# Kernel optimization log

Hardware: AMD Instinct MI355X
Metric: run time of the kernel (lower is better)

The kernel has to match this reference:

```python
import jax, jax.numpy as jnp
import numpy as np

H, Hk, Hv, Dk, Dv, K = 1536, 8, 16, 64, 64, 4
KEY_DIM = Hk * Dk            # 512
VALUE_DIM = Hv * Dv          # 1024
CONV_DIM = 2 * KEY_DIM + VALUE_DIM  # 2048


def setup_inputs() -> dict:
    key = jax.random.key(0)
    ks = jax.random.split(key, 12)
    s = 0.02
    return {
        "hidden_states": jax.random.normal(ks[0], (1, H, 1, 1), jnp.float32),
        "W_qkv": jax.random.normal(ks[1], (CONV_DIM, H), jnp.float32) * s,
        "W_z": jax.random.normal(ks[2], (VALUE_DIM, H), jnp.float32) * s,
        "W_a": jax.random.normal(ks[3], (Hv, H), jnp.float32) * s,
        "W_b": jax.random.normal(ks[4], (Hv, H), jnp.float32) * s,
        "W_out": jax.random.normal(ks[5], (H, VALUE_DIM), jnp.float32) * s,
        "conv1d_weight": jax.random.normal(ks[6], (CONV_DIM, K), jnp.float32) * 0.1,
        "A_log": jax.random.normal(ks[7], (Hv,), jnp.float32) * 0.1,
        "dt_bias": jax.random.normal(ks[8], (Hv,), jnp.float32) * 0.1,
        "norm_weight": jnp.ones((Dv,), jnp.float32),
        "state": jax.random.normal(ks[9], (1, Hv, Dk, Dv), jnp.float32) * 0.05,
        "conv_cache": jax.random.normal(ks[10], (1, CONV_DIM, K - 1), jnp.float32) * 0.1,
    }


def _l2n(t):
    # l2_normalize with eps=1e-12 (matches torch rsqrt(sum(x^2)+eps))
    return t * jax.lax.rsqrt(jnp.sum(t * t, axis=-1, keepdims=True) + 1e-12)


def reference(hidden_states, W_qkv, W_z, W_a, W_b, W_out, conv1d_weight,
              A_log, dt_bias, norm_weight, state, conv_cache):
    x = hidden_states.reshape(-1)                       # [H]
    qkv = W_qkv @ x                                     # [CONV_DIM]
    z = (W_z @ x).reshape(Hv, Dv)                       # gate, [Hv, Dv]
    a = W_a @ x                                         # [Hv]
    beta = jax.nn.sigmoid(W_b @ x)                      # [Hv]

    # causal conv as weighted sum over cache + current token
    combined = jnp.concatenate([conv_cache[0], qkv[:, None]], axis=1)  # [CONV_DIM, K]
    conv_out = jax.nn.silu(jnp.sum(combined * conv1d_weight, axis=1))  # [CONV_DIM]

    q = conv_out[:KEY_DIM].reshape(Hk, Dk)
    k = conv_out[KEY_DIM:2 * KEY_DIM].reshape(Hk, Dk)
    v = conv_out[2 * KEY_DIM:].reshape(Hv, Dv)

    rep = Hv // Hk                                      # kv_group = 2
    q = jnp.repeat(q, rep, axis=0)                      # [Hv, Dk]
    k = jnp.repeat(k, rep, axis=0)
    q = _l2n(q) * (Dk ** -0.5)
    k = _l2n(k)

    # gated decay
    g = -jnp.exp(A_log) * jax.nn.softplus(a + dt_bias)  # [Hv]
    st = state[0] * jnp.exp(g)[:, None, None]           # [Hv, Dk, Dv]

    # delta-rule update
    retrieved = jnp.einsum('hkv,hk->hv', st, k)         # [Hv, Dv]
    delta = (v - retrieved) * beta[:, None]             # [Hv, Dv]
    new_state = st + jnp.einsum('hk,hv->hkv', k, delta) # [Hv, Dk, Dv]

    out = jnp.einsum('hkv,hk->hv', new_state, q)        # [Hv, Dv]

    # gated RMSNorm over Dv
    var = jnp.mean(out * out, axis=-1, keepdims=True)
    out = norm_weight * (out * jax.lax.rsqrt(var + 1e-6)) * jax.nn.silu(z)

    y = W_out @ out.reshape(-1)                         # [H]
    return y.reshape(1, -1, 1, 1)
```

## Files before the change

### kernel.cpp

```cpp
#include <hip/hip_runtime.h>

#define H 1536
#define HK 8
#define HV 16
#define DK 64
#define DV 64
#define KEY_DIM 512
#define VALUE_DIM 1024
#define CONV_DIM 2048
#define NROWS1 (CONV_DIM + VALUE_DIM + HV + HV)
#define NBLK 256

__device__ unsigned g_ticket = 0;

__device__ __forceinline__ float wave_reduce_sum(float v) {
#pragma unroll
    for (int off = 32; off > 0; off >>= 1) v += __shfl_xor(v, off, 64);
    return v;
}

__device__ __forceinline__ float dot4(float4 a, float4 b) {
    return a.x * b.x + a.y * b.y + a.z * b.z + a.w * b.w;
}

__device__ __forceinline__ void grid_barrier() {
    __syncthreads();
    if (threadIdx.x == 0) {
        unsigned t = __hip_atomic_fetch_add(&g_ticket, 1u, __ATOMIC_ACQ_REL,
                                            __HIP_MEMORY_SCOPE_AGENT);
        unsigned target = (t / NBLK + 1u) * NBLK;
        while (__hip_atomic_load(&g_ticket, __ATOMIC_ACQUIRE,
                                 __HIP_MEMORY_SCOPE_AGENT) < target)
            __builtin_amdgcn_s_sleep(2);
    }
    __syncthreads();
}

__global__ __launch_bounds__(256) void fused_decode(
        const float* __restrict__ x,
        const float* __restrict__ Wqkv, const float* __restrict__ Wz,
        const float* __restrict__ Wa,   const float* __restrict__ Wb,
        const float* __restrict__ Wout,
        const float* __restrict__ conv_w, const float* __restrict__ conv_cache,
        const float* __restrict__ A_log, const float* __restrict__ dt_bias,
        const float* __restrict__ norm_w,
        const float* __restrict__ state,
        float* __restrict__ ws,
        float* __restrict__ og,
        float* __restrict__ y) {
    const int tid  = threadIdx.x;
    const int lane = tid & 63;
    const int wv   = tid >> 6;
    const int blk  = blockIdx.x;
    const int wg   = blk * 4 + wv;

    __shared__ float s_state[DK * DV];
    __shared__ float q_s[64], k_s[64], v_s[64];
    __shared__ float red_r[256], red_o[256];
    __shared__ float scal[3];

    if (blk < HV) {
        const float4* st4 = (const float4*)(state + (size_t)blk * DK * DV);
        float4* ss4 = (float4*)s_state;
#pragma unroll
        for (int j = 0; j < 4; ++j) ss4[tid + 256 * j] = st4[tid + 256 * j];
    }

    float4 wo0[4], wo1[4] = {};
    {
        const float4* w4 = (const float4*)(Wout + (size_t)wg * VALUE_DIM);
#pragma unroll
        for (int j = 0; j < 4; ++j) wo0[j] = w4[lane + 64 * j];
    }
    if (wg < 512) {
        const float4* w4 = (const float4*)(Wout + (size_t)(1024 + wg) * VALUE_DIM);
#pragma unroll
        for (int j = 0; j < 4; ++j) wo1[j] = w4[lane + 64 * j];
    }

    auto rowptr = [&](int row) -> const float* {
        if (row < CONV_DIM)                  return Wqkv + (size_t)row * H;
        if (row < CONV_DIM + VALUE_DIM)      return Wz + (size_t)(row - CONV_DIM) * H;
        if (row < CONV_DIM + VALUE_DIM + HV) return Wa + (size_t)(row - CONV_DIM - VALUE_DIM) * H;
        return Wb + (size_t)(row - CONV_DIM - VALUE_DIM - HV) * H;
    };
    const int r0 = wg * 3;
    const float4* wA = (const float4*)rowptr(r0);
    const float4* wB = (const float4*)rowptr(r0 + 1);
    const float4* wC = (const float4*)rowptr(r0 + 2);
    const bool extra = (wv == 0) && (blk >= 208) && (blk < 240);
    const int erow = 3072 + blk - 208;
    const float4* wD = (const float4*)rowptr(extra ? erow : r0);
    const float4* x4 = (const float4*)x;

    float a0 = 0.f, a1 = 0.f, a2 = 0.f, a3 = 0.f;
#pragma unroll
    for (int j = 0; j < 6; ++j) {
        const int idx = lane + 64 * j;
        const float4 xb = x4[idx];
        a0 += dot4(wA[idx], xb);
        a1 += dot4(wB[idx], xb);
        a2 += dot4(wC[idx], xb);
        if (extra) a3 += dot4(wD[idx], xb);
    }
    a0 = wave_reduce_sum(a0);
    a1 = wave_reduce_sum(a1);
    a2 = wave_reduce_sum(a2);
    if (lane == 0) { ws[r0] = a0; ws[r0 + 1] = a1; ws[r0 + 2] = a2; }
    if (extra) {
        a3 = wave_reduce_sum(a3);
        if (lane == 0) ws[erow] = a3;
    }

    grid_barrier();

    if (blk < HV) {
        const int h = blk;
        const int grp = wv;
        if (grp < 3) {
            int i;
            if (grp == 0)      i = (h >> 1) * 64 + lane;
            else if (grp == 1) i = KEY_DIM + (h >> 1) * 64 + lane;
            else               i = 2 * KEY_DIM + h * 64 + lane;
            float raw = conv_cache[i * 3 + 0] * conv_w[i * 4 + 0]
                      + conv_cache[i * 3 + 1] * conv_w[i * 4 + 1]
                      + conv_cache[i * 3 + 2] * conv_w[i * 4 + 2]
                      + ws[i]                 * conv_w[i * 4 + 3];
            float c = raw / (1.f + expf(-raw));
            if (grp == 2) {
                v_s[lane] = c;
            } else {
                float ss  = wave_reduce_sum(c * c);
                float inv = rsqrtf(ss + 1e-12f);
                if (grp == 0) q_s[lane] = c * inv * 0.125f;
                else          k_s[lane] = c * inv;
            }
        } else if (lane == 0) {
            float aa = ws[CONV_DIM + VALUE_DIM + h] + dt_bias[h];
            float sp = (aa > 20.f) ? aa : log1pf(expf(aa));
            scal[0] = expf(-expf(A_log[h]) * sp);
            float braw = ws[CONV_DIM + VALUE_DIM + HV + h];
            scal[1] = 1.f / (1.f + expf(-braw));
        }
        __syncthreads();

        float pr = 0.f, po = 0.f;
        const int k0 = grp * 16;
#pragma unroll
        for (int kk = 0; kk < 16; ++kk) {
            float s = s_state[(k0 + kk) * 64 + lane];
            pr += s * k_s[k0 + kk];
            po += s * q_s[k0 + kk];
        }
        red_r[tid] = pr;
        red_o[tid] = po;
        if (grp == 0) {
            float t = wave_reduce_sum(k_s[lane] * q_s[lane]);
            if (lane == 0) scal[2] = t;
        }
        __syncthreads();

        if (tid < 64) {
            const float decay = scal[0], beta = scal[1], kq = scal[2];
            float r = (red_r[tid] + red_r[64 + tid] + red_r[128 + tid] + red_r[192 + tid]) * decay;
            float o = (red_o[tid] + red_o[64 + tid] + red_o[128 + tid] + red_o[192 + tid]) * decay;
            float delta = (v_s[tid] - r) * beta;
            float outv  = o + delta * kq;
            float ss  = wave_reduce_sum(outv * outv);
            float inv = rsqrtf(ss * (1.f / 64.f) + 1e-6f);
            float zz  = ws[CONV_DIM + h * 64 + tid];
            float gate = zz / (1.f + expf(-zz));
            og[h * 64 + tid] = norm_w[tid] * outv * inv * gate;
        }
    }

    grid_barrier();

    const float4* og4 = (const float4*)og;
    const float4 g0 = og4[lane];
    const float4 g1 = og4[lane + 64];
    const float4 g2 = og4[lane + 128];
    const float4 g3 = og4[lane + 192];
    float acc = dot4(wo0[0], g0) + dot4(wo0[1], g1) + dot4(wo0[2], g2) + dot4(wo0[3], g3);
    acc = wave_reduce_sum(acc);
    if (lane == 0) y[wg] = acc;
    if (wg < 512) {
        float acc2 = dot4(wo1[0], g0) + dot4(wo1[1], g1) + dot4(wo1[2], g2) + dot4(wo1[3], g3);
        acc2 = wave_reduce_sum(acc2);
        if (lane == 0) y[1024 + wg] = acc2;
    }
}

extern "C" void kernel_launch(void* const* d_in, const int* in_sizes, int n_in,
                              void* d_out, int out_size, void* d_ws, size_t ws_size,
                              hipStream_t stream) {
    const float* x     = (const float*)d_in[0];
    const float* Wqkv  = (const float*)d_in[1];
    const float* Wz    = (const float*)d_in[2];
    const float* Wa    = (const float*)d_in[3];
    const float* Wb    = (const float*)d_in[4];
    const float* Wout  = (const float*)d_in[5];
    const float* convw = (const float*)d_in[6];
    const float* Alog  = (const float*)d_in[7];
    const float* dtb   = (const float*)d_in[8];
    const float* normw = (const float*)d_in[9];
    const float* state = (const float*)d_in[10];
    const float* cch   = (const float*)d_in[11];

    float* ws = (float*)d_ws;
    float* og = ws + NROWS1;
    float* y  = (float*)d_out;

    fused_decode<<<NBLK, 256, 0, stream>>>(x, Wqkv, Wz, Wa, Wb, Wout, convw, cch,
                                           Alog, dtb, normw, state, ws, og, y);
}
```

Before: 120.3 us.

## Split grid barrier into flag-based phases and move decode heads to tail blocks

Replaces the ticket-counter grid barrier with separate arrival counters and release flags. Only the 16 decode blocks wait for the first phase, while all blocks wait on a second flag that the decode blocks alone signal. The W_a and W_b projections move into the decode blocks, which now sit at the last 16 block indices, and their results stay in shared memory. All weight, x, conv and state loads are issued into registers before the dot products, to raise memory-level parallelism. This lowers barrier traffic and idle waiting, at the cost of more register pressure and an epoch scheme that relies on the counters' low bits lining up across launches.

```diff
diff --git a/kernel.cpp b/kernel.cpp
--- a/kernel.cpp
+++ b/kernel.cpp
@@ -8,35 +8,28 @@
 #define KEY_DIM 512
 #define VALUE_DIM 1024
 #define CONV_DIM 2048
-#define NROWS1 (CONV_DIM + VALUE_DIM + HV + HV)
+#define NROWS1 3104
 #define NBLK 256
-
-__device__ unsigned g_ticket = 0;
+#define DEC0 240
+
+struct BarrierState {
+    alignas(128) unsigned cnt1;
+    alignas(128) unsigned flag1;
+    alignas(128) unsigned cnt2;
+    alignas(128) unsigned flag2;
+};
+__device__ BarrierState g_bar;
 
 __device__ __forceinline__ float wave_reduce_sum(float v) {
 #pragma unroll
     for (int off = 32; off > 0; off >>= 1) v += __shfl_xor(v, off, 64);
     return v;
 }
-
 __device__ __forceinline__ float dot4(float4 a, float4 b) {
     return a.x * b.x + a.y * b.y + a.z * b.z + a.w * b.w;
 }
 
-__device__ __forceinline__ void grid_barrier() {
-    __syncthreads();
-    if (threadIdx.x == 0) {
-        unsigned t = __hip_atomic_fetch_add(&g_ticket, 1u, __ATOMIC_ACQ_REL,
-                                            __HIP_MEMORY_SCOPE_AGENT);
-        unsigned target = (t / NBLK + 1u) * NBLK;
-        while (__hip_atomic_load(&g_ticket, __ATOMIC_ACQUIRE,
-                                 __HIP_MEMORY_SCOPE_AGENT) < target)
-            __builtin_amdgcn_s_sleep(2);
-    }
-    __syncthreads();
-}
-
-__global__ __launch_bounds__(256) void fused_decode(
+__global__ __launch_bounds__(256, 1) void fused_decode(
         const float* __restrict__ x,
         const float* __restrict__ Wqkv, const float* __restrict__ Wz,
         const float* __restrict__ Wa,   const float* __restrict__ Wb,
@@ -53,99 +46,128 @@
     const int wv   = tid >> 6;
     const int blk  = blockIdx.x;
     const int wg   = blk * 4 + wv;
+    const int hblk = blk - DEC0;
+    const bool isdec = (hblk >= 0);
 
     __shared__ float s_state[DK * DV];
     __shared__ float q_s[64], k_s[64], v_s[64];
     __shared__ float red_r[256], red_o[256];
     __shared__ float scal[3];
-
-    if (blk < HV) {
-        const float4* st4 = (const float4*)(state + (size_t)blk * DK * DV);
-        float4* ss4 = (float4*)s_state;
-#pragma unroll
-        for (int j = 0; j < 4; ++j) ss4[tid + 256 * j] = st4[tid + 256 * j];
-    }
-
-    float4 wo0[4], wo1[4] = {};
+    __shared__ float s_ab[2];
+
+    const float4* x4 = (const float4*)x;
+    const int r0 = wg * 3;
+    const float4* wA = (const float4*)((r0   < CONV_DIM) ? Wqkv + (size_t)r0*H       : Wz + (size_t)(r0-CONV_DIM)*H);
+    const float4* wB = (const float4*)((r0+1 < CONV_DIM) ? Wqkv + (size_t)(r0+1)*H   : Wz + (size_t)(r0+1-CONV_DIM)*H);
+    const float4* wC = (const float4*)((r0+2 < CONV_DIM) ? Wqkv + (size_t)(r0+2)*H   : Wz + (size_t)(r0+2-CONV_DIM)*H);
+
+    float4 rx[6], rA[6], rB[6], rC[6];
+#pragma unroll
+    for (int j = 0; j < 6; ++j) rx[j] = x4[lane + 64*j];
+#pragma unroll
+    for (int j = 0; j < 6; ++j) rA[j] = wA[lane + 64*j];
+#pragma unroll
+    for (int j = 0; j < 6; ++j) rB[j] = wB[lane + 64*j];
+#pragma unroll
+    for (int j = 0; j < 6; ++j) rC[j] = wC[lane + 64*j];
+
+    float4 wo0[4], wo1[4];
     {
         const float4* w4 = (const float4*)(Wout + (size_t)wg * VALUE_DIM);
 #pragma unroll
-        for (int j = 0; j < 4; ++j) wo0[j] = w4[lane + 64 * j];
+        for (int j = 0; j < 4; ++j) wo0[j] = w4[lane + 64*j];
     }
     if (wg < 512) {
         const float4* w4 = (const float4*)(Wout + (size_t)(1024 + wg) * VALUE_DIM);
 #pragma unroll
-        for (int j = 0; j < 4; ++j) wo1[j] = w4[lane + 64 * j];
-    }
-
-    auto rowptr = [&](int row) -> const float* {
-        if (row < CONV_DIM)                  return Wqkv + (size_t)row * H;
-        if (row < CONV_DIM + VALUE_DIM)      return Wz + (size_t)(row - CONV_DIM) * H;
-        if (row < CONV_DIM + VALUE_DIM + HV) return Wa + (size_t)(row - CONV_DIM - VALUE_DIM) * H;
-        return Wb + (size_t)(row - CONV_DIM - VALUE_DIM - HV) * H;
-    };
-    const int r0 = wg * 3;
-    const float4* wA = (const float4*)rowptr(r0);
-    const float4* wB = (const float4*)rowptr(r0 + 1);
-    const float4* wC = (const float4*)rowptr(r0 + 2);
-    const bool extra = (wv == 0) && (blk >= 208) && (blk < 240);
-    const int erow = 3072 + blk - 208;
-    const float4* wD = (const float4*)rowptr(extra ? erow : r0);
-    const float4* x4 = (const float4*)x;
-
-    float a0 = 0.f, a1 = 0.f, a2 = 0.f, a3 = 0.f;
+        for (int j = 0; j < 4; ++j) wo1[j] = w4[lane + 64*j];
+    }
+
+    float4 rAB[6];
+    const bool abwave = isdec && (wv < 2);
+    if (abwave) {
+        const float4* w4 = (const float4*)(((wv == 0) ? Wa : Wb) + (size_t)hblk * H);
+#pragma unroll
+        for (int j = 0; j < 6; ++j) rAB[j] = w4[lane + 64*j];
+    }
+    float pre = 0.f, w3 = 0.f;
+    int qkvrow = 0;
+    if (isdec && wv < 3) {
+        if (wv == 0)      qkvrow = (hblk >> 1) * 64 + lane;
+        else if (wv == 1) qkvrow = KEY_DIM + (hblk >> 1) * 64 + lane;
+        else              qkvrow = 2 * KEY_DIM + hblk * 64 + lane;
+        pre = conv_cache[qkvrow*3+0] * conv_w[qkvrow*4+0]
+            + conv_cache[qkvrow*3+1] * conv_w[qkvrow*4+1]
+            + conv_cache[qkvrow*3+2] * conv_w[qkvrow*4+2];
+        w3  = conv_w[qkvrow*4+3];
+    }
+    float r_alog = 0.f, r_dtb = 0.f;
+    if (isdec && wv == 3 && lane == 0) { r_alog = A_log[hblk]; r_dtb = dt_bias[hblk]; }
+    if (isdec) {
+        const float4* st4 = (const float4*)(state + (size_t)hblk * DK * DV);
+        float4* ss4 = (float4*)s_state;
+#pragma unroll
+        for (int j = 0; j < 4; ++j) ss4[tid + 256*j] = st4[tid + 256*j];
+    }
+
+    float a0 = 0.f, a1 = 0.f, a2 = 0.f;
 #pragma unroll
     for (int j = 0; j < 6; ++j) {
-        const int idx = lane + 64 * j;
-        const float4 xb = x4[idx];
-        a0 += dot4(wA[idx], xb);
-        a1 += dot4(wB[idx], xb);
-        a2 += dot4(wC[idx], xb);
-        if (extra) a3 += dot4(wD[idx], xb);
+        a0 += dot4(rA[j], rx[j]);
+        a1 += dot4(rB[j], rx[j]);
+        a2 += dot4(rC[j], rx[j]);
     }
     a0 = wave_reduce_sum(a0);
     a1 = wave_reduce_sum(a1);
     a2 = wave_reduce_sum(a2);
-    if (lane == 0) { ws[r0] = a0; ws[r0 + 1] = a1; ws[r0 + 2] = a2; }
-    if (extra) {
-        a3 = wave_reduce_sum(a3);
-        if (lane == 0) ws[erow] = a3;
-    }
-
-    grid_barrier();
-
-    if (blk < HV) {
-        const int h = blk;
-        const int grp = wv;
-        if (grp < 3) {
-            int i;
-            if (grp == 0)      i = (h >> 1) * 64 + lane;
-            else if (grp == 1) i = KEY_DIM + (h >> 1) * 64 + lane;
-            else               i = 2 * KEY_DIM + h * 64 + lane;
-            float raw = conv_cache[i * 3 + 0] * conv_w[i * 4 + 0]
-                      + conv_cache[i * 3 + 1] * conv_w[i * 4 + 1]
-                      + conv_cache[i * 3 + 2] * conv_w[i * 4 + 2]
-                      + ws[i]                 * conv_w[i * 4 + 3];
+    if (lane == 0) { ws[r0] = a0; ws[r0+1] = a1; ws[r0+2] = a2; }
+    if (abwave) {
+        float ab = 0.f;
+#pragma unroll
+        for (int j = 0; j < 6; ++j) ab += dot4(rAB[j], rx[j]);
+        ab = wave_reduce_sum(ab);
+        if (lane == 0) s_ab[wv] = ab;
+    }
+
+    __syncthreads();
+    unsigned ep = 0;
+    if (tid == 0) {
+        unsigned t = __hip_atomic_fetch_add(&g_bar.cnt1, 1u, __ATOMIC_ACQ_REL,
+                                            __HIP_MEMORY_SCOPE_AGENT);
+        ep = t >> 8;
+        if ((t & 255u) == 255u)
+            __hip_atomic_store(&g_bar.flag1, ep + 1u, __ATOMIC_RELEASE,
+                               __HIP_MEMORY_SCOPE_AGENT);
+    }
+
+    if (isdec) {
+        if (tid == 0) {
+            while (__hip_atomic_load(&g_bar.flag1, __ATOMIC_ACQUIRE,
+                                     __HIP_MEMORY_SCOPE_AGENT) <= ep)
+                __builtin_amdgcn_s_sleep(8);
+        }
+        __syncthreads();
+
+        if (wv < 3) {
+            float raw = pre + ws[qkvrow] * w3;
             float c = raw / (1.f + expf(-raw));
-            if (grp == 2) {
-                v_s[lane] = c;
-            } else {
-                float ss  = wave_reduce_sum(c * c);
-                float inv = rsqrtf(ss + 1e-12f);
-                if (grp == 0) q_s[lane] = c * inv * 0.125f;
-                else          k_s[lane] = c * inv;
+            if (wv == 2) v_s[lane] = c;
+            else {
+                float ssum = wave_reduce_sum(c * c);
+                float inv = rsqrtf(ssum + 1e-12f);
+                if (wv == 0) q_s[lane] = c * inv * 0.125f;
+                else         k_s[lane] = c * inv;
             }
         } else if (lane == 0) {
-            float aa = ws[CONV_DIM + VALUE_DIM + h] + dt_bias[h];
+            float aa = s_ab[0] + r_dtb;
             float sp = (aa > 20.f) ? aa : log1pf(expf(aa));
-            scal[0] = expf(-expf(A_log[h]) * sp);
-            float braw = ws[CONV_DIM + VALUE_DIM + HV + h];
-            scal[1] = 1.f / (1.f + expf(-braw));
+            scal[0] = expf(-expf(r_alog) * sp);
+            scal[1] = 1.f / (1.f + expf(-s_ab[1]));
         }
         __syncthreads();
 
         float pr = 0.f, po = 0.f;
-        const int k0 = grp * 16;
+        const int k0 = wv * 16;
 #pragma unroll
         for (int kk = 0; kk < 16; ++kk) {
             float s = s_state[(k0 + kk) * 64 + lane];
@@ -154,7 +176,7 @@
         }
         red_r[tid] = pr;
         red_o[tid] = po;
-        if (grp == 0) {
+        if (wv == 0) {
             float t = wave_reduce_sum(k_s[lane] * q_s[lane]);
             if (lane == 0) scal[2] = t;
         }
@@ -162,19 +184,32 @@
 
         if (tid < 64) {
             const float decay = scal[0], beta = scal[1], kq = scal[2];
-            float r = (red_r[tid] + red_r[64 + tid] + red_r[128 + tid] + red_r[192 + tid]) * decay;
-            float o = (red_o[tid] + red_o[64 + tid] + red_o[128 + tid] + red_o[192 + tid]) * decay;
+            float r = (red_r[tid] + red_r[64+tid] + red_r[128+tid] + red_r[192+tid]) * decay;
+            float o = (red_o[tid] + red_o[64+tid] + red_o[128+tid] + red_o[192+tid]) * decay;
             float delta = (v_s[tid] - r) * beta;
             float outv  = o + delta * kq;
-            float ss  = wave_reduce_sum(outv * outv);
-            float inv = rsqrtf(ss * (1.f / 64.f) + 1e-6f);
-            float zz  = ws[CONV_DIM + h * 64 + tid];
+            float ssum = wave_reduce_sum(outv * outv);
+            float inv = rsqrtf(ssum * (1.f / 64.f) + 1e-6f);
+            float zz  = ws[CONV_DIM + hblk * 64 + tid];
             float gate = zz / (1.f + expf(-zz));
-            og[h * 64 + tid] = norm_w[tid] * outv * inv * gate;
-        }
-    }
-
-    grid_barrier();
+            og[hblk * 64 + tid] = norm_w[tid] * outv * inv * gate;
+        }
+        __syncthreads();
+        if (tid == 0) {
+            unsigned t2 = __hip_atomic_fetch_add(&g_bar.cnt2, 1u, __ATOMIC_ACQ_REL,
+                                                 __HIP_MEMORY_SCOPE_AGENT);
+            if ((t2 & 15u) == 15u)
+                __hip_atomic_store(&g_bar.flag2, (t2 >> 4) + 1u, __ATOMIC_RELEASE,
+                                   __HIP_MEMORY_SCOPE_AGENT);
+        }
+    }
+
+    if (tid == 0) {
+        while (__hip_atomic_load(&g_bar.flag2, __ATOMIC_ACQUIRE,
+                                 __HIP_MEMORY_SCOPE_AGENT) <= ep)
+            __builtin_amdgcn_s_sleep(16);
+    }
+    __syncthreads();
 
     const float4* og4 = (const float4*)og;
     const float4 g0 = og4[lane];
```

After: 123.4 us. 1.03x slower.
